# Optimization experiments

Measured on AMD Instinct MI355X. Metric: run time of the kernel, lower is better.

The kernel has to match this reference:

```python
import jax, jax.numpy as jnp
import numpy as np
from jax import lax

C_IN, C_OUT, LEVEL = 64, 128, 4
SOFTMAX_SCALE = 10.0
ESCAPE_NAN = 1e-4


def conv3(x, w, b):
    y = lax.conv_general_dilated(x, w, (1, 1), [(1, 1), (1, 1)],
                                 dimension_numbers=('NCHW', 'OIHW', 'NCHW'))
    return y + b[None, :, None, None]


def conv1(x, w, b):  # 1x1 conv, w: [O, I]
    return jnp.einsum('oi,bihw->bohw', w, x) + b[None, :, None, None]


def prelu(x, a):
    return jnp.where(x >= 0, x, a * x)


def resblock(x, w1, b1, w2, b2):  # EDSR ResBlock, res_scale=1
    return x + conv3(jax.nn.relu(conv3(x, w1, b1)), w2, b2)


def patches9(x):
    # 3x3 'same' (zero-pad 1) patches: [B,C,H,W] -> [B,C,3,3,H*W], (C,kh,kw) order like torch unfold
    B, C, H, W = x.shape
    xp = jnp.pad(x, ((0, 0), (0, 0), (1, 1), (1, 1)))
    p = jnp.stack([xp[:, :, i:i + H, j:j + W] for i in range(3) for j in range(3)], axis=2)
    return p.reshape(B, C, 3, 3, H * W)


def pyramid_attention(x, mbw, mbb, mba, mw, mb_, ma, aw, ab, aa):
    B, C, H, W = x.shape
    C2 = C // 2
    scales = [1.0 - i / 10 for i in range(LEVEL)]
    match_base = prelu(conv1(x, mbw, mbb), mba)            # [B,C2,H,W]
    xp = patches9(match_base).reshape(B, C2 * 9, H * W)    # query patches (same-padded input to conv2d)
    w_all, rw_all = [], []
    for s in scales:
        if s != 1.0:
            Hs, Ws = int(H * s), int(W * s)
            ref = jax.image.resize(x, (B, C, Hs, Ws), method='bilinear')
        else:
            ref = x
        base = prelu(conv1(ref, aw, ab), aa)               # conv_assembly: [B,C,Hs,Ws]
        rw_all.append(jnp.transpose(patches9(base), (0, 4, 1, 2, 3)))   # [B,L,C,3,3]
        refm = prelu(conv1(ref, mw, mb_), ma)              # conv_match:    [B,C2,Hs,Ws]
        w_all.append(jnp.transpose(patches9(refm), (0, 4, 1, 2, 3)))    # [B,L,C2,3,3]
    wi = jnp.concatenate(w_all, axis=1)                    # [B,Lt,C2,3,3]
    rw = jnp.concatenate(rw_all, axis=1)                   # [B,Lt,C,3,3]
    Lt = wi.shape[1]
    norm = jnp.maximum(jnp.sqrt(jnp.sum(wi * wi, axis=(2, 3, 4), keepdims=True)), ESCAPE_NAN)
    wn = (wi / norm).reshape(B, Lt, C2 * 9)
    # conv2d-as-correlation: scores[b,l,p] = <patch_p(match_base_b), wn[b,l]>
    scores = jnp.einsum('blk,bkp->blp', wn, xp)            # [B,Lt,H*W]
    att = jax.nn.softmax(scores * SOFTMAX_SCALE, axis=1).reshape(B, Lt, H, W)

    def tconv(y, rw_b):  # conv_transpose2d(stride=1, padding=1) == conv with swapped+flipped kernel
        wk = jnp.flip(jnp.transpose(rw_b, (1, 0, 2, 3)), axis=(2, 3))  # [C,Lt,3,3]
        return lax.conv_general_dilated(y[None], wk, (1, 1), [(1, 1), (1, 1)],
                                        dimension_numbers=('NCHW', 'OIHW', 'NCHW'))[0]

    out = jax.vmap(tconv)(att, rw) / 4.0
    return out + x  # res_scale = 1


def reference(x, bb0_w, bb0_b, bb0_a, rb1_w1, rb1_b1, rb1_w2, rb1_b2,
              pamb_w, pamb_b, pamb_a, pam_w, pam_b, pam_a, paa_w, paa_b, paa_a,
              rb2_w1, rb2_b1, rb2_w2, rb2_b2):
    h = lax.reduce_window(x, -jnp.inf, lax.max, (1, 1, 2, 2), (1, 1, 2, 2), 'VALID')  # MaxPool2d(2)
    h = prelu(conv3(h, bb0_w, bb0_b), bb0_a)               # BasicBlock in->out
    h = resblock(h, rb1_w1, rb1_b1, rb1_w2, rb1_b2)
    h = pyramid_attention(h, pamb_w, pamb_b, pamb_a, pam_w, pam_b, pam_a, paa_w, paa_b, paa_a)
    h = resblock(h, rb2_w1, rb2_b1, rb2_w2, rb2_b2)
    return h


def setup_inputs() -> dict:
    key = jax.random.key(0)
    ks = jax.random.split(key, 20)
    B, H, W = 2, 128, 128
    Ci, Co = C_IN, C_OUT
    C2 = Co // 2

    def n(k, shape, s=0.05):
        return jax.random.normal(k, shape, jnp.float32) * s

    a = jnp.asarray(0.25, jnp.float32)  # PReLU default init
    return {
        'x': jax.random.normal(ks[0], (B, Ci, H, W), jnp.float32),
        'bb0_w': n(ks[1], (Co, Ci, 3, 3)), 'bb0_b': n(ks[2], (Co,)), 'bb0_a': a,
        'rb1_w1': n(ks[3], (Co, Co, 3, 3)), 'rb1_b1': n(ks[4], (Co,)),
        'rb1_w2': n(ks[5], (Co, Co, 3, 3)), 'rb1_b2': n(ks[6], (Co,)),
        'pamb_w': n(ks[7], (C2, Co)), 'pamb_b': n(ks[8], (C2,)), 'pamb_a': a,
        'pam_w': n(ks[9], (C2, Co)), 'pam_b': n(ks[10], (C2,)), 'pam_a': a,
        'paa_w': n(ks[11], (Co, Co)), 'paa_b': n(ks[12], (Co,)), 'paa_a': a,
        'rb2_w1': n(ks[13], (Co, Co, 3, 3)), 'rb2_b1': n(ks[14], (Co,)),
        'rb2_w2': n(ks[15], (Co, Co, 3, 3)), 'rb2_b2': n(ks[16], (Co,)),
    }
```

## Files before the change

### kernel.cpp

```cpp
#include <hip/hip_runtime.h>

typedef unsigned short u16;
typedef __attribute__((ext_vector_type(8))) __bf16 bf16x8;
typedef __attribute__((ext_vector_type(8))) unsigned short ushort8;
typedef __attribute__((ext_vector_type(4))) float f32x4;

__device__ __forceinline__ float bf2f(u16 u) { return __uint_as_float(((unsigned)u) << 16); }
__device__ __forceinline__ u16 f2bf(float f) {
    unsigned x = __float_as_uint(f);
    x += 0x7fffu + ((x >> 16) & 1u);
    return (u16)(x >> 16);
}
__device__ __forceinline__ u16 f2h16(float f) {
    _Float16 h = (_Float16)f; u16 r; __builtin_memcpy(&r, &h, 2); return r;
}
__device__ __forceinline__ float h162f(u16 u) {
    _Float16 h; __builtin_memcpy(&h, &u, 2); return (float)h;
}

#define LP 13824

__global__ __launch_bounds__(256) void d7_gemm(
    const u16* __restrict__ A, const u16* __restrict__ B,
    int N, int K, int kLen, int mTiles, int S,
    long aBS, long bBS,
    const float* __restrict__ bias, const float* __restrict__ alpha, int act,
    const float* __restrict__ resid, long residBS,
    float* __restrict__ outF, long oFBS,
    u16* __restrict__ outB, long oBBS,
    u16* __restrict__ outT, int ldT, long oTBS,
    float* __restrict__ outP, long pMN, int pBf)
{
    __shared__ u16 As[128 * 40];
    __shared__ u16 Bs[128 * 40];

    const int tid = threadIdx.x;
    const int wv = tid >> 6, lane = tid & 63;
    const int wm = wv >> 1, wn = wv & 1;
    const int bn = blockIdx.x;
    const int bm = blockIdx.y % mTiles;
    const int ks = blockIdx.y / mTiles;
    const int z  = blockIdx.z;
    const int kStart = ks * kLen;

    const int srow = tid >> 1;
    const int soff = (tid & 1) * 16;
    const u16* gA = A + z * aBS + (size_t)(bm * 128 + srow) * K + kStart + soff;
    const u16* gB = B + z * bBS + (size_t)(bn * 128 + srow) * K + kStart + soff;
    u16* lA = &As[srow * 40 + soff];
    u16* lB = &Bs[srow * 40 + soff];

    f32x4 acc[4][4] = {};

    for (int k0 = 0; k0 < kLen; k0 += 32) {
        __syncthreads();
        ((uint4*)lA)[0] = ((const uint4*)gA)[0];
        ((uint4*)lA)[1] = ((const uint4*)gA)[1];
        ((uint4*)lB)[0] = ((const uint4*)gB)[0];
        ((uint4*)lB)[1] = ((const uint4*)gB)[1];
        gA += 32; gB += 32;
        __syncthreads();

        bf16x8 a[4], b[4];
        #pragma unroll
        for (int mt = 0; mt < 4; ++mt)
            a[mt] = *reinterpret_cast<const bf16x8*>(&As[(wm * 64 + mt * 16 + (lane & 15)) * 40 + (lane >> 4) * 8]);
        #pragma unroll
        for (int nt = 0; nt < 4; ++nt)
            b[nt] = *reinterpret_cast<const bf16x8*>(&Bs[(wn * 64 + nt * 16 + (lane & 15)) * 40 + (lane >> 4) * 8]);
        #pragma unroll
        for (int mt = 0; mt < 4; ++mt)
            #pragma unroll
            for (int nt = 0; nt < 4; ++nt)
                acc[mt][nt] = __builtin_amdgcn_mfma_f32_16x16x32_bf16(a[mt], b[nt], acc[mt][nt], 0, 0, 0);
    }

    if (outP) {
        const size_t pbase = ((size_t)z * S + ks) * pMN;
        #pragma unroll
        for (int mt = 0; mt < 4; ++mt) {
            const int mg = bm * 128 + wm * 64 + mt * 16 + ((lane >> 4) << 2);
            #pragma unroll
            for (int nt = 0; nt < 4; ++nt) {
                const int ng = bn * 128 + wn * 64 + nt * 16 + (lane & 15);
                if (pBf) {
                    u16* pp = (u16*)outP + pbase;
                    #pragma unroll
                    for (int r = 0; r < 4; ++r)
                        pp[(size_t)(mg + r) * N + ng] = f2bf(acc[mt][nt][r]);
                } else {
                    float* pp = outP + pbase;
                    #pragma unroll
                    for (int r = 0; r < 4; ++r)
                        pp[(size_t)(mg + r) * N + ng] = acc[mt][nt][r];
                }
            }
        }
        return;
    }

    const float avalS = (act == 1) ? alpha[0] : 0.0f;
    #pragma unroll
    for (int mt = 0; mt < 4; ++mt) {
        const int mg = bm * 128 + wm * 64 + mt * 16 + ((lane >> 4) << 2);
        float bv[4] = {0.f, 0.f, 0.f, 0.f}, av[4];
        if (bias) {
            #pragma unroll
            for (int r = 0; r < 4; ++r) bv[r] = bias[mg + r];
        }
        if (act == 3) {
            #pragma unroll
            for (int r = 0; r < 4; ++r) av[r] = alpha[mg + r];
        }
        #pragma unroll
        for (int nt = 0; nt < 4; ++nt) {
            const int ng = bn * 128 + wn * 64 + nt * 16 + (lane & 15);
            float v[4];
            #pragma unroll
            for (int r = 0; r < 4; ++r) {
                float t = acc[mt][nt][r] + bv[r];
                if (act == 1) t = (t >= 0.f) ? t : avalS * t;
                else if (act == 2) t = fmaxf(t, 0.f);
                else if (act == 3) t = (t >= 0.f) ? t : av[r] * t;
                if (resid) t += resid[z * residBS + (size_t)(mg + r) * N + ng];
                v[r] = t;
            }
            if (outF) {
                #pragma unroll
                for (int r = 0; r < 4; ++r) outF[z * oFBS + (size_t)(mg + r) * N + ng] = v[r];
            }
            if (outB) {
                #pragma unroll
                for (int r = 0; r < 4; ++r) outB[z * oBBS + (size_t)(mg + r) * N + ng] = f2bf(v[r]);
            }
            if (outT) {
                unsigned long long pk = (unsigned long long)f2bf(v[0])
                    | ((unsigned long long)f2bf(v[1]) << 16)
                    | ((unsigned long long)f2bf(v[2]) << 32)
                    | ((unsigned long long)f2bf(v[3]) << 48);
                *reinterpret_cast<unsigned long long*>(outT + z * oTBS + (size_t)ng * ldT + mg) = pk;
            }
        }
    }
}

__global__ __launch_bounds__(256) void d7_epi(
    const void* __restrict__ parts, int S, long sStride, long bStride,
    const float* __restrict__ bias, const float* __restrict__ alpha, int act,
    const float* __restrict__ resid, long residBS, float scale,
    float* __restrict__ out, long outBS, int total, int pBf)
{
    int i = blockIdx.x * 256 + threadIdx.x;
    if (i >= total) return;
    int b = blockIdx.z;
    float s = 0.f;
    if (pBf) {
        const u16* p = (const u16*)parts + b * bStride + i;
        for (int t = 0; t < S; ++t) s += bf2f(p[(size_t)t * sStride]);
    } else {
        const float* p = (const float*)parts + b * bStride + i;
        for (int t = 0; t < S; ++t) s += p[(size_t)t * sStride];
    }
    s *= scale;
    if (bias) s += bias[i >> 12];
    if (act == 1) { float a = alpha[0]; s = (s >= 0.f) ? s : a * s; }
    else if (act == 2) s = fmaxf(s, 0.f);
    if (resid) s += resid[b * residBS + i];
    out[b * outBS + i] = s;
}

__global__ __launch_bounds__(256) void d7_cast(const float* __restrict__ src, u16* __restrict__ dst, int n) {
    int i = blockIdx.x * 256 + threadIdx.x;
    if (i < n) dst[i] = f2bf(src[i]);
}

__global__ __launch_bounds__(256) void d7_wbuild(
    const float* __restrict__ pamb_w, const float* __restrict__ pam_w, const float* __restrict__ paa_w,
    const float* __restrict__ pamb_b, const float* __restrict__ pam_b, const float* __restrict__ paa_b,
    const float* __restrict__ pamb_a, const float* __restrict__ pam_a, const float* __restrict__ paa_a,
    u16* __restrict__ W1, u16* __restrict__ W2,
    float* __restrict__ b1, float* __restrict__ a1,
    float* __restrict__ b2, float* __restrict__ a2)
{
    int i = blockIdx.x * 256 + threadIdx.x;
    if (i < 256 * 128) {
        int r = i >> 7, c = i & 127;
        float w1 = (r < 64) ? pamb_w[r * 128 + c] : (r < 128) ? pam_w[(r - 64) * 128 + c] : paa_w[(r - 128) * 128 + c];
        W1[i] = f2bf(w1);
        float w2 = (r < 64) ? pam_w[r * 128 + c] : (r < 192) ? paa_w[(r - 64) * 128 + c] : 0.f;
        W2[i] = f2bf(w2);
    }
    if (i < 256) {
        int r = i;
        b1[r] = (r < 64) ? pamb_b[r] : (r < 128) ? pam_b[r - 64] : paa_b[r - 128];
        a1[r] = (r < 64) ? pamb_a[0] : (r < 128) ? pam_a[0] : paa_a[0];
        b2[r] = (r < 64) ? pam_b[r] : (r < 192) ? paa_b[r - 64] : 0.f;
        a2[r] = (r < 64) ? pam_a[0] : (r < 192) ? paa_a[0] : 0.f;
    }
}

__global__ __launch_bounds__(256) void d7_maxpool(const float* __restrict__ x, float* __restrict__ out) {
    int p = blockIdx.x * 256 + threadIdx.x;
    int c = blockIdx.y, b = blockIdx.z;
    int oh = p >> 6, ow = p & 63;
    const float* ip = x + ((size_t)b * 64 + c) * 16384;
    float v0 = ip[(2 * oh) * 128 + 2 * ow];
    float v1 = ip[(2 * oh) * 128 + 2 * ow + 1];
    float v2 = ip[(2 * oh + 1) * 128 + 2 * ow];
    float v3 = ip[(2 * oh + 1) * 128 + 2 * ow + 1];
    out[((size_t)b * 64 + c) * 4096 + p] = fmaxf(fmaxf(v0, v1), fmaxf(v2, v3));
}

__global__ __launch_bounds__(256) void d7_im2col(const float* __restrict__ img, u16* __restrict__ patT,
                                                 int Cin, long inBS, long outBS) {
    int K = Cin * 9;
    int k = blockIdx.x * 256 + threadIdx.x;
    if (k >= K) return;
    int p = blockIdx.y, b = blockIdx.z;
    int c = k / 9, k9 = k - c * 9;
    int h = p >> 6, w = p & 63;
    int y = h + k9 / 3 - 1, x = w + (k9 % 3) - 1;
    const float* ip = img + b * inBS;
    float v = (y >= 0 && y < 64 && x >= 0 && x < 64) ? ip[(size_t)c * 4096 + y * 64 + x] : 0.f;
    patT[b * outBS + (size_t)p * K + k] = f2bf(v);
}

__global__ __launch_bounds__(256) void d7_t32(const float* __restrict__ in, long inBS, int P,
                                              u16* __restrict__ out, long outBS) {
    __shared__ float tile[32][33];
    int p0 = blockIdx.x * 32, c0 = blockIdx.y * 32, b = blockIdx.z;
    int tx = threadIdx.x & 31, ty = threadIdx.x >> 5;
    const float* ip = in + b * inBS;
    #pragma unroll
    for (int i = 0; i < 32; i += 8) {
        int c = c0 + ty + i, p = p0 + tx;
        tile[ty + i][tx] = (p < P) ? ip[(size_t)c * P + p] : 0.f;
    }
    __syncthreads();
    u16* op = out + b * outBS;
    #pragma unroll
    for (int i = 0; i < 32; i += 8) {
        int p = p0 + ty + i, c = c0 + tx;
        if (p < P) op[(size_t)p * 128 + c] = f2bf(tile[tx][ty + i]);
    }
}

__global__ __launch_bounds__(256) void d7_scK(const u16* __restrict__ cT, long cBS, int ldC, int colBase,
                                              int pOff, int P, int HS, int Wp, int off,
                                              u16* __restrict__ dst, long dBS,
                                              float* __restrict__ s2out) {
    int t = blockIdx.x * 256 + threadIdx.x;
    int p = t >> 3, cg = t & 7;
    if (p >= P) return;
    int b = blockIdx.z;
    ushort8 v = *reinterpret_cast<const ushort8*>(cT + b * cBS + (size_t)(pOff + p) * ldC + colBase + cg * 8);
    int h = p / HS, w = p - h * HS;
    int lp = off + (h + 1) * Wp + w + 1;
    *reinterpret_cast<ushort8*>(dst + b * dBS + (size_t)lp * 64 + cg * 8) = v;
    if (s2out) {
        float ss = 0.f;
        #pragma unroll
        for (int i = 0; i < 8; ++i) { float f = bf2f(v[i]); ss += f * f; }
        ss += __shfl_xor(ss, 1);
        ss += __shfl_xor(ss, 2);
        ss += __shfl_xor(ss, 4);
        if (cg == 0) s2out[(size_t)b * LP + lp] = ss;
    }
}

__global__ __launch_bounds__(256) void d7_scR(const u16* __restrict__ cO, long cBS, int ldC, int rowBase,
                                              int pOff, int P, int HS, int Wp, int off,
                                              u16* __restrict__ dst, long dBS) {
    int p = blockIdx.x * 256 + threadIdx.x;
    if (p >= P) return;
    int co = blockIdx.y, b = blockIdx.z;
    u16 v = cO[b * cBS + (size_t)(rowBase + co) * ldC + pOff + p];
    int h = p / HS, w = p - h * HS;
    int lp = off + (h + 1) * Wp + w + 1;
    dst[b * dBS + (size_t)co * LP + lp] = v;
}

template <int OS>
__device__ __forceinline__ void d7_taps(int o, int& i0, float w3[3]) {
    const float inv = 64.0f / OS;
    float s = (o + 0.5f) * inv - 0.5f;
    i0 = (int)ceilf(s - inv);
    float wsum = 0.f;
    #pragma unroll
    for (int t = 0; t < 3; ++t) {
        int y = i0 + t;
        float wt = 1.0f - fabsf((float)y - s) / inv;
        wt = (wt > 0.f && y >= 0 && y < 64) ? wt : 0.f;
        w3[t] = wt; wsum += wt;
    }
    float r = 1.0f / wsum;
    w3[0] *= r; w3[1] *= r; w3[2] *= r;
}

template <int OS>
__global__ __launch_bounds__(256) void d7_resize(const float* __restrict__ in, float* __restrict__ out, long out_bs) {
    int p = blockIdx.x * 256 + threadIdx.x;
    if (p >= OS * OS) return;
    int c = blockIdx.y, b = blockIdx.z;
    int oh = p / OS, ow = p - oh * OS;
    const float* img = in + ((size_t)b * 128 + c) * 4096;
    int y0, x0; float wy[3], wx[3];
    d7_taps<OS>(oh, y0, wy);
    d7_taps<OS>(ow, x0, wx);
    float sum = 0.f;
    #pragma unroll
    for (int iy = 0; iy < 3; ++iy) {
        if (wy[iy] <= 0.f) continue;
        float rs = 0.f;
        #pragma unroll
        for (int ix = 0; ix < 3; ++ix) {
            if (wx[ix] <= 0.f) continue;
            rs += wx[ix] * img[(y0 + iy) * 64 + (x0 + ix)];
        }
        sum += wy[iy] * rs;
    }
    out[(size_t)b * out_bs + (size_t)c * OS * OS + p] = sum;
}

__device__ __forceinline__ int d7_scaleW(int l) {
    return (l < 4752) ? 72 : (l < 8528) ? 64 : (l < 11496) ? 56 : 48;
}

__global__ __launch_bounds__(256) void d7_rnormk(const float* __restrict__ s2, float* __restrict__ rnorm) {
    int l = blockIdx.x * 256 + threadIdx.x;
    if (l >= LP) return;
    int zb = blockIdx.z;
    int off, W, HS;
    if (l < 4752)       { off = 0;     W = 72; HS = 64; }
    else if (l < 8528)  { off = 4752;  W = 64; HS = 57; }
    else if (l < 11496) { off = 8528;  W = 56; HS = 51; }
    else                { off = 11496; W = 48; HS = 44; }
    int li = l - off, y = li / W, x = li - y * W;
    float v = 0.f;
    if (y >= 1 && y <= HS && x >= 1 && x <= HS) {
        const float* s = s2 + (size_t)zb * LP;
        float a = 0.f;
        #pragma unroll
        for (int dy = -1; dy <= 1; ++dy)
            #pragma unroll
            for (int dx = -1; dx <= 1; ++dx)
                a += s[l + dy * W + dx];
        v = 14.426950408889634f / fmaxf(sqrtf(a), 1e-4f);
    }
    rnorm[(size_t)zb * LP + l] = v;
}

__global__ __launch_bounds__(256) void d7_st1(const u16* __restrict__ in, u16* __restrict__ out,
                                              const float* __restrict__ rnorm) {
    int vg = blockIdx.x * 256 + threadIdx.x;
    if (vg >= LP / 8) return;
    int l8 = vg << 3;
    int p = blockIdx.y;
    int h = p >> 6, w = p & 63;
    int W = d7_scaleW(l8);
    float acc[8] = {0.f, 0.f, 0.f, 0.f, 0.f, 0.f, 0.f, 0.f};
    #pragma unroll
    for (int a = -1; a <= 1; ++a) {
        int ph = h + a;
        if ((unsigned)ph >= 64u) continue;
        #pragma unroll
        for (int b = -1; b <= 1; ++b) {
            int pw = w + b;
            if ((unsigned)pw >= 64u) continue;
            const u16* rp = in + (size_t)(p + a * 64 + b) * LP + l8 + a * W;
            ushort8 v = *reinterpret_cast<const ushort8*>(rp);
            if (b == 0) {
                #pragma unroll
                for (int i = 0; i < 8; ++i) acc[i] += bf2f(v[i]);
            } else if (b == -1) {
                acc[0] += bf2f(rp[-1]);
                #pragma unroll
                for (int i = 1; i < 8; ++i) acc[i] += bf2f(v[i - 1]);
            } else {
                acc[7] += bf2f(rp[8]);
                #pragma unroll
                for (int i = 0; i < 7; ++i) acc[i] += bf2f(v[i + 1]);
            }
        }
    }
    const float4 rn0 = *reinterpret_cast<const float4*>(rnorm + l8);
    const float4 rn1 = *reinterpret_cast<const float4*>(rnorm + l8 + 4);
    float rn[8] = {rn0.x, rn0.y, rn0.z, rn0.w, rn1.x, rn1.y, rn1.z, rn1.w};
    ushort8 res;
    #pragma unroll
    for (int i = 0; i < 8; ++i)
        res[i] = f2h16((rn[i] != 0.f) ? acc[i] * rn[i] : -1e4f);
    *reinterpret_cast<ushort8*>(out + (size_t)p * LP + l8) = res;
}

__global__ __launch_bounds__(256) void d7_stats(const u16* __restrict__ sc, float* __restrict__ statM) {
    int p = blockIdx.x, tid = threadIdx.x, wv = tid >> 6, lane = tid & 63;
    const u16* row = sc + (size_t)p * LP;
    float m = -3e38f;
    #pragma unroll
    for (int it = 0; it < 7; ++it) {
        int vg = tid + it * 256;
        if (vg < LP / 8) {
            ushort8 v = *reinterpret_cast<const ushort8*>(row + vg * 8);
            #pragma unroll
            for (int i = 0; i < 8; ++i) m = fmaxf(m, h162f(v[i]));
        }
    }
    #pragma unroll
    for (int o = 1; o < 64; o <<= 1) m = fmaxf(m, __shfl_xor(m, o));
    __shared__ float red[4];
    if (lane == 0) red[wv] = m;
    __syncthreads();
    m = fmaxf(fmaxf(red[0], red[1]), fmaxf(red[2], red[3]));
    __syncthreads();
    float s = 0.f;
    #pragma unroll
    for (int it = 0; it < 7; ++it) {
        int vg = tid + it * 256;
        if (vg < LP / 8) {
            ushort8 v = *reinterpret_cast<const ushort8*>(row + vg * 8);
            #pragma unroll
            for (int i = 0; i < 8; ++i) s += __builtin_amdgcn_exp2f(h162f(v[i]) - m);
        }
    }
    #pragma unroll
    for (int o = 1; o < 64; o <<= 1) s += __shfl_xor(s, o);
    if (lane == 0) red[wv] = s;
    __syncthreads();
    if (tid == 0) {
        float Z = red[0] + red[1] + red[2] + red[3];
        statM[p] = m + __log2f(Z);
    }
}

__global__ __launch_bounds__(256) void d7_st2(const u16* __restrict__ in,
                                              const float* __restrict__ statM,
                                              const float* __restrict__ rnorm,
                                              u16* __restrict__ out) {
    int vg = blockIdx.x * 256 + threadIdx.x;
    if (vg >= LP / 8) return;
    int l8 = vg << 3;
    int p = blockIdx.y;
    int h = p >> 6, w = p & 63;
    int W = d7_scaleW(l8);
    float acc[8] = {0.f, 0.f, 0.f, 0.f, 0.f, 0.f, 0.f, 0.f};
    #pragma unroll
    for (int a = -1; a <= 1; ++a) {
        int ph = h + a;
        if ((unsigned)ph >= 64u) continue;
        #pragma unroll
        for (int b = -1; b <= 1; ++b) {
            int pw = w + b;
            if ((unsigned)pw >= 64u) continue;
            int r = p + a * 64 + b;
            float M = statM[r];
            const u16* rp = in + (size_t)r * LP + l8 + a * W;
            ushort8 v = *reinterpret_cast<const ushort8*>(rp);
            if (b == 0) {
                #pragma unroll
                for (int i = 0; i < 8; ++i) acc[i] += __builtin_amdgcn_exp2f(h162f(v[i]) - M);
            } else if (b == -1) {
                acc[0] += __builtin_amdgcn_exp2f(h162f(rp[-1]) - M);
                #pragma unroll
                for (int i = 1; i < 8; ++i) acc[i] += __builtin_amdgcn_exp2f(h162f(v[i - 1]) - M);
            } else {
                acc[7] += __builtin_amdgcn_exp2f(h162f(rp[8]) - M);
                #pragma unroll
                for (int i = 0; i < 7; ++i) acc[i] += __builtin_amdgcn_exp2f(h162f(v[i + 1]) - M);
            }
        }
    }
    const float4 rn0 = *reinterpret_cast<const float4*>(rnorm + l8);
    const float4 rn1 = *reinterpret_cast<const float4*>(rnorm + l8 + 4);
    float rn[8] = {rn0.x, rn0.y, rn0.z, rn0.w, rn1.x, rn1.y, rn1.z, rn1.w};
    ushort8 res;
    #pragma unroll
    for (int i = 0; i < 8; ++i)
        res[i] = f2bf((rn[i] != 0.f) ? acc[i] : 0.f);
    *reinterpret_cast<ushort8*>(out + (size_t)p * LP + l8) = res;
}

extern "C" void kernel_launch(void* const* d_in, const int* in_sizes, int n_in,
                              void* d_out, int out_size, void* d_ws, size_t ws_size,
                              hipStream_t stream) {
    const float* x      = (const float*)d_in[0];
    const float* bb0_w  = (const float*)d_in[1];
    const float* bb0_b  = (const float*)d_in[2];
    const float* bb0_a  = (const float*)d_in[3];
    const float* rb1_w1 = (const float*)d_in[4];
    const float* rb1_b1 = (const float*)d_in[5];
    const float* rb1_w2 = (const float*)d_in[6];
    const float* rb1_b2 = (const float*)d_in[7];
    const float* pamb_w = (const float*)d_in[8];
    const float* pamb_b = (const float*)d_in[9];
    const float* pamb_a = (const float*)d_in[10];
    const float* pam_w  = (const float*)d_in[11];
    const float* pam_b  = (const float*)d_in[12];
    const float* pam_a  = (const float*)d_in[13];
    const float* paa_w  = (const float*)d_in[14];
    const float* paa_b  = (const float*)d_in[15];
    const float* paa_a  = (const float*)d_in[16];
    const float* rb2_w1 = (const float*)d_in[17];
    const float* rb2_b1 = (const float*)d_in[18];
    const float* rb2_w2 = (const float*)d_in[19];
    const float* rb2_b2 = (const float*)d_in[20];
    float* out = (float*)d_out;
    (void)in_sizes; (void)n_in; (void)out_size; (void)ws_size;

    char* wp = (char*)d_ws;
    auto alloc = [&](size_t nbytes) { void* p = wp; wp += (nbytes + 255) & ~(size_t)255; return p; };
    const size_t BIG = 4096ull * LP * 2;
    char* big1r  = (char*)alloc(BIG + 1024);
    char* big2r  = (char*)alloc(BIG + 1024);
    float* h0f   = (float*)alloc(2ull * 64 * 4096 * 4);
    float* h1f   = (float*)alloc(2ull * 128 * 4096 * 4);
    float* h2f   = (float*)alloc(2ull * 128 * 4096 * 4);
    float* paf   = (float*)alloc(2ull * 128 * 4096 * 4);
    float* tbuf  = (float*)alloc(2ull * 128 * 4096 * 4);
    u16* mbT     = (u16*)alloc(2ull * 4096 * 64 * 2);
    u16* refmT   = (u16*)alloc(2ull * LP * 64 * 2);
    u16* baseA   = (u16*)alloc(2ull * 128 * LP * 2);
    float* s2b   = (float*)alloc(2ull * LP * 4);
    float* rnorm = (float*)alloc(2ull * LP * 4);
    float* statM = (float*)alloc(4096ull * 4);
    u16* W1      = (u16*)alloc(256ull * 128 * 2);
    u16* W2      = (u16*)alloc(256ull * 128 * 2);
    float* b1v   = (float*)alloc(256 * 4);
    float* a1v   = (float*)alloc(256 * 4);
    float* b2v   = (float*)alloc(256 * 4);
    float* a2v   = (float*)alloc(256 * 4);
    u16* A0      = (u16*)alloc(73728ull * 2);
    u16* A1      = (u16*)alloc(147456ull * 2);
    u16* A2      = (u16*)alloc(147456ull * 2);
    u16* A3      = (u16*)alloc(147456ull * 2);
    u16* A4      = (u16*)alloc(147456ull * 2);
    u16* patT    = (u16*)big1r;
    u16* h2T     = (u16*)big1r;
    u16* refbT   = (u16*)(big1r + (4ull << 20));
    u16* S0T     = (u16*)(big1r + 512);
    u16* gT      = (u16*)(big1r + 512);
    float* parts = (float*)big2r;
    u16* cT1     = (u16*)big2r;
    u16* cOut1   = (u16*)(big2r + (4ull << 20));
    u16* cT2     = (u16*)(big2r + (8ull << 20));
    u16* cOut2   = (u16*)(big2r + (16ull << 20));
    float* refb  = (float*)(big2r + (26ull << 20));
    u16* scT     = (u16*)(big2r + 512);

    const long h2bs = 128L * 4096;
    const long pMN = 128L * 4096;
    const long refbs = 128L * 7786;
    const long mbTbs = 4096L * 64, rmTbs = (long)LP * 64, baBS = 128L * LP;
    const long cT1bs = 4096L * 256, cO1bs = 256L * 4096;
    const long cT2bs = 7808L * 256, cO2bs = 256L * 7808;
    const long rbTbs = 7808L * 128;

    auto conv = [&](const float* src, const u16* W, int Cin, const float* bias,
                    const float* alpha, int act, const float* resid, float* dst) {
        int K = Cin * 9;
        d7_im2col<<<dim3((K + 255) / 256, 4096, 2), 256, 0, stream>>>(src, patT, Cin, (long)Cin * 4096, 4096L * K);
        d7_gemm<<<dim3(32, 6, 2), 256, 0, stream>>>(W, patT, 4096, K, K / 6, 1, 6,
            0, 4096L * K, nullptr, nullptr, 0, nullptr, 0,
            nullptr, 0, nullptr, 0, nullptr, 0, 0, parts, pMN, 0);
        d7_epi<<<dim3(2048, 1, 2), 256, 0, stream>>>(parts, 6, pMN, 6 * pMN,
            bias, alpha, act, resid, h2bs, 1.0f, dst, h2bs, (int)pMN, 0);
    };

    d7_cast<<<dim3(288), 256, 0, stream>>>(bb0_w, A0, 73728);
    d7_cast<<<dim3(576), 256, 0, stream>>>(rb1_w1, A1, 147456);
    d7_cast<<<dim3(576), 256, 0, stream>>>(rb1_w2, A2, 147456);
    d7_cast<<<dim3(576), 256, 0, stream>>>(rb2_w1, A3, 147456);
    d7_cast<<<dim3(576), 256, 0, stream>>>(rb2_w2, A4, 147456);
    d7_wbuild<<<dim3(128), 256, 0, stream>>>(pamb_w, pam_w, paa_w, pamb_b, pam_b, paa_b,
                                             pamb_a, pam_a, paa_a, W1, W2, b1v, a1v, b2v, a2v);

    d7_maxpool<<<dim3(16, 64, 2), 256, 0, stream>>>(x, h0f);
    conv(h0f, A0, 64, bb0_b, bb0_a, 1, nullptr, h1f);
    conv(h1f, A1, 128, rb1_b1, nullptr, 2, nullptr, tbuf);
    conv(tbuf, A2, 128, rb1_b2, nullptr, 0, h1f, h2f);

    d7_resize<57><<<dim3(13, 128, 2), 256, 0, stream>>>(h2f, refb, refbs);
    d7_resize<51><<<dim3(11, 128, 2), 256, 0, stream>>>(h2f, refb + 3249L * 128, refbs);
    d7_resize<44><<<dim3(8, 128, 2), 256, 0, stream>>>(h2f, refb + 5850L * 128, refbs);

    hipMemsetAsync(refbT, 0, 2ull * rbTbs * 2, stream);
    d7_t32<<<dim3(128, 4, 2), 256, 0, stream>>>(h2f, h2bs, 4096, h2T, 4096L * 128);
    d7_t32<<<dim3(102, 4, 2), 256, 0, stream>>>(refb, refbs, 3249, refbT, rbTbs);
    d7_t32<<<dim3(82, 4, 2), 256, 0, stream>>>(refb + 3249L * 128, refbs, 2601, refbT + 3249L * 128, rbTbs);
    d7_t32<<<dim3(61, 4, 2), 256, 0, stream>>>(refb + 5850L * 128, refbs, 1936, refbT + 5850L * 128, rbTbs);

    d7_gemm<<<dim3(32, 2, 2), 256, 0, stream>>>(W1, h2T, 4096, 128, 128, 2, 1,
        0, 4096L * 128, b1v, a1v, 3, nullptr, 0,
        nullptr, 0, cOut1, cO1bs, cT1, 256, cT1bs, nullptr, 0, 0);
    d7_gemm<<<dim3(61, 2, 2), 256, 0, stream>>>(W2, refbT, 7808, 128, 128, 2, 1,
        0, rbTbs, b2v, a2v, 3, nullptr, 0,
        nullptr, 0, cOut2, cO2bs, cT2, 256, cT2bs, nullptr, 0, 0);

    hipMemsetAsync(refmT, 0, 2ull * LP * 64 * 2, stream);
    hipMemsetAsync(baseA, 0, 2ull * 128 * LP * 2, stream);
    hipMemsetAsync(s2b, 0, 2ull * LP * 4, stream);
    d7_scK<<<dim3(128, 1, 2), 256, 0, stream>>>(cT1, cT1bs, 256, 0, 0, 4096, 64, 64, -65, mbT, mbTbs, nullptr);
    d7_scK<<<dim3(128, 1, 2), 256, 0, stream>>>(cT1, cT1bs, 256, 64, 0, 4096, 64, 72, 0, refmT, rmTbs, s2b);
    d7_scK<<<dim3(102, 1, 2), 256, 0, stream>>>(cT2, cT2bs, 256, 0, 0, 3249, 57, 64, 4752, refmT, rmTbs, s2b);
    d7_scK<<<dim3(82, 1, 2), 256, 0, stream>>>(cT2, cT2bs, 256, 0, 3249, 2601, 51, 56, 8528, refmT, rmTbs, s2b);
    d7_scK<<<dim3(61, 1, 2), 256, 0, stream>>>(cT2, cT2bs, 256, 0, 5850, 1936, 44, 48, 11496, refmT, rmTbs, s2b);
    d7_scR<<<dim3(16, 128, 2), 256, 0, stream>>>(cOut1, cO1bs, 4096, 128, 0, 4096, 64, 72, 0, baseA, baBS);
    d7_scR<<<dim3(13, 128, 2), 256, 0, stream>>>(cOut2, cO2bs, 7808, 64, 0, 3249, 57, 64, 4752, baseA, baBS);
    d7_scR<<<dim3(11, 128, 2), 256, 0, stream>>>(cOut2, cO2bs, 7808, 64, 3249, 2601, 51, 56, 8528, baseA, baBS);
    d7_scR<<<dim3(8, 128, 2), 256, 0, stream>>>(cOut2, cO2bs, 7808, 64, 5850, 1936, 44, 48, 11496, baseA, baBS);

    d7_rnormk<<<dim3(54, 1, 2), 256, 0, stream>>>(s2b, rnorm);

    for (int b = 0; b < 2; ++b) {
        d7_gemm<<<dim3(32, 108, 1), 256, 0, stream>>>(refmT + b * rmTbs, mbT + b * mbTbs,
            4096, 64, 64, 108, 1, 0, 0, nullptr, nullptr, 0, nullptr, 0,
            nullptr, 0, nullptr, 0, S0T, LP, 0, nullptr, 0, 0);
        d7_st1<<<dim3(7, 4096), 256, 0, stream>>>(S0T, scT, rnorm + (size_t)b * LP);
        d7_stats<<<dim3(4096), 256, 0, stream>>>(scT, statM);
        d7_st2<<<dim3(7, 4096), 256, 0, stream>>>(scT, statM, rnorm + (size_t)b * LP, gT);
        d7_gemm<<<dim3(32, 12, 1), 256, 0, stream>>>(baseA + b * baBS, gT,
            4096, LP, LP / 12, 1, 12, 0, 0, nullptr, nullptr, 0, nullptr, 0,
            nullptr, 0, nullptr, 0, nullptr, 0, 0, parts, pMN, 1);
        d7_epi<<<dim3(2048, 1, 1), 256, 0, stream>>>(parts, 12, pMN, 0,
            nullptr, nullptr, 0, h2f + b * h2bs, 0, 0.25f, paf + b * h2bs, 0, (int)pMN, 1);
    }

    conv(paf, A3, 128, rb2_b1, nullptr, 2, nullptr, tbuf);
    conv(tbuf, A4, 128, rb2_b2, nullptr, 0, paf, out);
}
```

Baseline: 993.5 us.

## Fuse score smoothing with softmax stats and use lane shuffles for halo reads

Merges the 3x3 diagonal smoothing kernel (st1) and the row max/log-sum-exp stats kernel into one block-per-row kernel. Each row's fp16 scores stay in registers between the passes, so the separate stats pass no longer re-reads them from memory. In both smoothing kernels the unaligned neighbour element for the ±1 column shift now comes from a lane shuffle, with a scalar load only at wavefront edges. The max now skips masked entries, and the conv path's gemm/epilogue last flag changes from 0 to 1, which may alter precision or layout. The fused kernel launches one block per row instead of seven, so parallelism and occupancy per row drop.

```diff
diff --git a/kernel.cpp b/kernel.cpp
--- a/kernel.cpp
+++ b/kernel.cpp
@@ -350,66 +350,66 @@
     rnorm[(size_t)zb * LP + l] = v;
 }
 
-__global__ __launch_bounds__(256) void d7_st1(const u16* __restrict__ in, u16* __restrict__ out,
-                                              const float* __restrict__ rnorm) {
-    int vg = blockIdx.x * 256 + threadIdx.x;
-    if (vg >= LP / 8) return;
-    int l8 = vg << 3;
-    int p = blockIdx.y;
-    int h = p >> 6, w = p & 63;
-    int W = d7_scaleW(l8);
-    float acc[8] = {0.f, 0.f, 0.f, 0.f, 0.f, 0.f, 0.f, 0.f};
-    #pragma unroll
-    for (int a = -1; a <= 1; ++a) {
-        int ph = h + a;
-        if ((unsigned)ph >= 64u) continue;
-        #pragma unroll
-        for (int b = -1; b <= 1; ++b) {
-            int pw = w + b;
-            if ((unsigned)pw >= 64u) continue;
-            const u16* rp = in + (size_t)(p + a * 64 + b) * LP + l8 + a * W;
-            ushort8 v = *reinterpret_cast<const ushort8*>(rp);
-            if (b == 0) {
+__global__ __launch_bounds__(256) void d7_st1f(const u16* __restrict__ in, u16* __restrict__ out,
+                                               const float* __restrict__ rnorm,
+                                               float* __restrict__ statM) {
+    const int p = blockIdx.x;
+    const int tid = threadIdx.x, wvi = tid >> 6, lane = tid & 63;
+    const int h = p >> 6, w = p & 63;
+    ushort8 vals16[7];
+    float m = -3e38f;
+    #pragma unroll
+    for (int it = 0; it < 7; ++it) {
+        int vg = tid + it * 256;
+        if (vg >= LP / 8) continue;
+        int l8 = vg << 3;
+        int W = d7_scaleW(l8);
+        float acc[8] = {0.f, 0.f, 0.f, 0.f, 0.f, 0.f, 0.f, 0.f};
+        #pragma unroll
+        for (int a = -1; a <= 1; ++a) {
+            int ph = h + a;
+            if ((unsigned)ph >= 64u) continue;
+            const u16* rb = in + (size_t)(p + a * 64) * LP + l8 + a * W;
+            {
+                ushort8 v = *reinterpret_cast<const ushort8*>(rb);
                 #pragma unroll
                 for (int i = 0; i < 8; ++i) acc[i] += bf2f(v[i]);
-            } else if (b == -1) {
-                acc[0] += bf2f(rp[-1]);
+            }
+            if (w - 1 >= 0) {
+                const u16* r1 = rb - LP;
+                ushort8 v = *reinterpret_cast<const ushort8*>(r1);
+                int up = __shfl_up((int)v[7], 1);
+                u16 e = (lane == 0) ? r1[-1] : (u16)up;
+                acc[0] += bf2f(e);
                 #pragma unroll
                 for (int i = 1; i < 8; ++i) acc[i] += bf2f(v[i - 1]);
-            } else {
-                acc[7] += bf2f(rp[8]);
+            }
+            if (w + 1 < 64) {
+                const u16* r1 = rb + LP;
+                ushort8 v = *reinterpret_cast<const ushort8*>(r1);
+                int dn = __shfl_down((int)v[0], 1);
+                u16 e = (lane == 63) ? r1[8] : (u16)dn;
                 #pragma unroll
                 for (int i = 0; i < 7; ++i) acc[i] += bf2f(v[i + 1]);
-            }
-        }
-    }
-    const float4 rn0 = *reinterpret_cast<const float4*>(rnorm + l8);
-    const float4 rn1 = *reinterpret_cast<const float4*>(rnorm + l8 + 4);
-    float rn[8] = {rn0.x, rn0.y, rn0.z, rn0.w, rn1.x, rn1.y, rn1.z, rn1.w};
-    ushort8 res;
-    #pragma unroll
-    for (int i = 0; i < 8; ++i)
-        res[i] = f2h16((rn[i] != 0.f) ? acc[i] * rn[i] : -1e4f);
-    *reinterpret_cast<ushort8*>(out + (size_t)p * LP + l8) = res;
-}
-
-__global__ __launch_bounds__(256) void d7_stats(const u16* __restrict__ sc, float* __restrict__ statM) {
-    int p = blockIdx.x, tid = threadIdx.x, wv = tid >> 6, lane = tid & 63;
-    const u16* row = sc + (size_t)p * LP;
-    float m = -3e38f;
-    #pragma unroll
-    for (int it = 0; it < 7; ++it) {
-        int vg = tid + it * 256;
-        if (vg < LP / 8) {
-            ushort8 v = *reinterpret_cast<const ushort8*>(row + vg * 8);
-            #pragma unroll
-            for (int i = 0; i < 8; ++i) m = fmaxf(m, h162f(v[i]));
-        }
+                acc[7] += bf2f(e);
+            }
+        }
+        const float4 rn0 = *reinterpret_cast<const float4*>(rnorm + l8);
+        const float4 rn1 = *reinterpret_cast<const float4*>(rnorm + l8 + 4);
+        float rn[8] = {rn0.x, rn0.y, rn0.z, rn0.w, rn1.x, rn1.y, rn1.z, rn1.w};
+        ushort8 res;
+        #pragma unroll
+        for (int i = 0; i < 8; ++i) {
+            float val = (rn[i] != 0.f) ? acc[i] * rn[i] : -1e4f;
+            res[i] = f2h16(val);
+            if (rn[i] != 0.f) m = fmaxf(m, val);
+        }
+        vals16[it] = res;
     }
     #pragma unroll
     for (int o = 1; o < 64; o <<= 1) m = fmaxf(m, __shfl_xor(m, o));
     __shared__ float red[4];
-    if (lane == 0) red[wv] = m;
+    if (lane == 0) red[wvi] = m;
     __syncthreads();
     m = fmaxf(fmaxf(red[0], red[1]), fmaxf(red[2], red[3]));
     __syncthreads();
@@ -417,19 +417,24 @@
     #pragma unroll
     for (int it = 0; it < 7; ++it) {
         int vg = tid + it * 256;
-        if (vg < LP / 8) {
-            ushort8 v = *reinterpret_cast<const ushort8*>(row + vg * 8);
-            #pragma unroll
-            for (int i = 0; i < 8; ++i) s += __builtin_amdgcn_exp2f(h162f(v[i]) - m);
-        }
+        if (vg >= LP / 8) continue;
+        ushort8 res = vals16[it];
+        #pragma unroll
+        for (int i = 0; i < 8; ++i) s += __builtin_amdgcn_exp2f(h162f(res[i]) - m);
     }
     #pragma unroll
     for (int o = 1; o < 64; o <<= 1) s += __shfl_xor(s, o);
-    if (lane == 0) red[wv] = s;
+    if (lane == 0) red[wvi] = s;
     __syncthreads();
     if (tid == 0) {
         float Z = red[0] + red[1] + red[2] + red[3];
         statM[p] = m + __log2f(Z);
+    }
+    #pragma unroll
+    for (int it = 0; it < 7; ++it) {
+        int vg = tid + it * 256;
+        if (vg >= LP / 8) continue;
+        *reinterpret_cast<ushort8*>(out + (size_t)p * LP + (vg << 3)) = vals16[it];
     }
 }
 
@@ -439,6 +444,7 @@
                                               u16* __restrict__ out) {
     int vg = blockIdx.x * 256 + threadIdx.x;
     if (vg >= LP / 8) return;
+    const int lane = threadIdx.x & 63;
     int l8 = vg << 3;
     int p = blockIdx.y;
     int h = p >> 6, w = p & 63;
@@ -448,26 +454,32 @@
     for (int a = -1; a <= 1; ++a) {
         int ph = h + a;
         if ((unsigned)ph >= 64u) continue;
-        #pragma unroll
-        for (int b = -1; b <= 1; ++b) {
-            int pw = w + b;
-            if ((unsigned)pw >= 64u) continue;
-            int r = p + a * 64 + b;
-            float M = statM[r];
-            const u16* rp = in + (size_t)r * LP + l8 + a * W;
-            ushort8 v = *reinterpret_cast<const ushort8*>(rp);
-            if (b == 0) {
-                #pragma unroll
-                for (int i = 0; i < 8; ++i) acc[i] += __builtin_amdgcn_exp2f(h162f(v[i]) - M);
-            } else if (b == -1) {
-                acc[0] += __builtin_amdgcn_exp2f(h162f(rp[-1]) - M);
-                #pragma unroll
-                for (int i = 1; i < 8; ++i) acc[i] += __builtin_amdgcn_exp2f(h162f(v[i - 1]) - M);
-            } else {
-                acc[7] += __builtin_amdgcn_exp2f(h162f(rp[8]) - M);
-                #pragma unroll
-                for (int i = 0; i < 7; ++i) acc[i] += __builtin_amdgcn_exp2f(h162f(v[i + 1]) - M);
-            }
+        const u16* rb = in + (size_t)(p + a * 64) * LP + l8 + a * W;
+        {
+            float M = statM[p + a * 64];
+            ushort8 v = *reinterpret_cast<const ushort8*>(rb);
+            #pragma unroll
+            for (int i = 0; i < 8; ++i) acc[i] += __builtin_amdgcn_exp2f(h162f(v[i]) - M);
+        }
+        if (w - 1 >= 0) {
+            float M = statM[p + a * 64 - 1];
+            const u16* r1 = rb - LP;
+            ushort8 v = *reinterpret_cast<const ushort8*>(r1);
+            int up = __shfl_up((int)v[7], 1);
+            u16 e = (lane == 0) ? r1[-1] : (u16)up;
+            acc[0] += __builtin_amdgcn_exp2f(h162f(e) - M);
+            #pragma unroll
+            for (int i = 1; i < 8; ++i) acc[i] += __builtin_amdgcn_exp2f(h162f(v[i - 1]) - M);
+        }
+        if (w + 1 < 64) {
+            float M = statM[p + a * 64 + 1];
+            const u16* r1 = rb + LP;
+            ushort8 v = *reinterpret_cast<const ushort8*>(r1);
+            int dn = __shfl_down((int)v[0], 1);
+            u16 e = (lane == 63) ? r1[8] : (u16)dn;
+            #pragma unroll
+            for (int i = 0; i < 7; ++i) acc[i] += __builtin_amdgcn_exp2f(h162f(v[i + 1]) - M);
+            acc[7] += __builtin_amdgcn_exp2f(h162f(e) - M);
         }
     }
     const float4 rn0 = *reinterpret_cast<const float4*>(rnorm + l8);
@@ -561,9 +573,9 @@
         d7_im2col<<<dim3((K + 255) / 256, 4096, 2), 256, 0, stream>>>(src, patT, Cin, (long)Cin * 4096, 4096L * K);
         d7_gemm<<<dim3(32, 6, 2), 256, 0, stream>>>(W, patT, 4096, K, K / 6, 1, 6,
             0, 4096L * K, nullptr, nullptr, 0, nullptr, 0,
-            nullptr, 0, nullptr, 0, nullptr, 0, 0, parts, pMN, 0);
+            nullptr, 0, nullptr, 0, nullptr, 0, 0, parts, pMN, 1);
         d7_epi<<<dim3(2048, 1, 2), 256, 0, stream>>>(parts, 6, pMN, 6 * pMN,
-            bias, alpha, act, resid, h2bs, 1.0f, dst, h2bs, (int)pMN, 0);
+            bias, alpha, act, resid, h2bs, 1.0f, dst, h2bs, (int)pMN, 1);
     };
 
     d7_cast<<<dim3(288), 256, 0, stream>>>(bb0_w, A0, 73728);
@@ -615,8 +627,7 @@
         d7_gemm<<<dim3(32, 108, 1), 256, 0, stream>>>(refmT + b * rmTbs, mbT + b * mbTbs,
             4096, 64, 64, 108, 1, 0, 0, nullptr, nullptr, 0, nullptr, 0,
             nullptr, 0, nullptr, 0, S0T, LP, 0, nullptr, 0, 0);
-        d7_st1<<<dim3(7, 4096), 256, 0, stream>>>(S0T, scT, rnorm + (size_t)b * LP);
-        d7_stats<<<dim3(4096), 256, 0, stream>>>(scT, statM);
+        d7_st1f<<<dim3(4096), 256, 0, stream>>>(S0T, scT, rnorm + (size_t)b * LP, statM);
         d7_st2<<<dim3(7, 4096), 256, 0, stream>>>(scT, statM, rnorm + (size_t)b * LP, gT);
         d7_gemm<<<dim3(32, 12, 1), 256, 0, stream>>>(baseA + b * baBS, gT,
             4096, LP, LP / 12, 1, 12, 0, 0, nullptr, nullptr, 0, nullptr, 0,
```

Result: slower. 1.035 ms (+4.1%).

## Fuse softmax row stats into score stencil kernel with partial combine

Applied to the files above, without the earlier changes.

The per-row max and sum-exp statistics are now computed inside d7_st1 from values already in registers, writing per-block partials that a small d7_comb kernel merges. This removes the separate d7_stats pass that re-read the full score matrix twice per batch. The horizontal-neighbour loads in the stencil are replaced by wave shuffles of neighbouring lanes' vectors, cutting redundant global reads. Buffer offsets and padding are enlarged, and a gemm/epilogue mode flag for the convs is switched, which may change that path's behaviour.

```diff
diff --git a/kernel.cpp b/kernel.cpp
--- a/kernel.cpp
+++ b/kernel.cpp
@@ -351,86 +351,99 @@
 }
 
 __global__ __launch_bounds__(256) void d7_st1(const u16* __restrict__ in, u16* __restrict__ out,
-                                              const float* __restrict__ rnorm) {
-    int vg = blockIdx.x * 256 + threadIdx.x;
-    if (vg >= LP / 8) return;
+                                              const float* __restrict__ rnorm,
+                                              float2* __restrict__ part) {
+    const int tid = threadIdx.x, wvi = tid >> 6, lane = tid & 63;
+    int vg = blockIdx.x * 256 + tid;
+    const bool active = vg < LP / 8;
     int l8 = vg << 3;
     int p = blockIdx.y;
     int h = p >> 6, w = p & 63;
-    int W = d7_scaleW(l8);
-    float acc[8] = {0.f, 0.f, 0.f, 0.f, 0.f, 0.f, 0.f, 0.f};
-    #pragma unroll
-    for (int a = -1; a <= 1; ++a) {
-        int ph = h + a;
-        if ((unsigned)ph >= 64u) continue;
-        #pragma unroll
-        for (int b = -1; b <= 1; ++b) {
-            int pw = w + b;
-            if ((unsigned)pw >= 64u) continue;
-            const u16* rp = in + (size_t)(p + a * 64 + b) * LP + l8 + a * W;
-            ushort8 v = *reinterpret_cast<const ushort8*>(rp);
-            if (b == 0) {
+    float vals[8];
+    if (active) {
+        int W = d7_scaleW(l8);
+        float acc[8] = {0.f, 0.f, 0.f, 0.f, 0.f, 0.f, 0.f, 0.f};
+        #pragma unroll
+        for (int a = -1; a <= 1; ++a) {
+            int ph = h + a;
+            if ((unsigned)ph >= 64u) continue;
+            const u16* rb = in + (size_t)(p + a * 64) * LP + l8 + a * W;
+            {
+                ushort8 v = *reinterpret_cast<const ushort8*>(rb);
                 #pragma unroll
                 for (int i = 0; i < 8; ++i) acc[i] += bf2f(v[i]);
-            } else if (b == -1) {
-                acc[0] += bf2f(rp[-1]);
+            }
+            if (w - 1 >= 0) {
+                const u16* r1 = rb - LP;
+                ushort8 v = *reinterpret_cast<const ushort8*>(r1);
+                int up = __shfl_up((int)v[7], 1);
+                u16 e = (lane == 0) ? r1[-1] : (u16)up;
+                acc[0] += bf2f(e);
                 #pragma unroll
                 for (int i = 1; i < 8; ++i) acc[i] += bf2f(v[i - 1]);
-            } else {
-                acc[7] += bf2f(rp[8]);
+            }
+            if (w + 1 < 64) {
+                const u16* r1 = rb + LP;
+                ushort8 v = *reinterpret_cast<const ushort8*>(r1);
+                int dn = __shfl_down((int)v[0], 1);
+                u16 e = (lane == 63) ? r1[8] : (u16)dn;
                 #pragma unroll
                 for (int i = 0; i < 7; ++i) acc[i] += bf2f(v[i + 1]);
-            }
-        }
-    }
-    const float4 rn0 = *reinterpret_cast<const float4*>(rnorm + l8);
-    const float4 rn1 = *reinterpret_cast<const float4*>(rnorm + l8 + 4);
-    float rn[8] = {rn0.x, rn0.y, rn0.z, rn0.w, rn1.x, rn1.y, rn1.z, rn1.w};
-    ushort8 res;
-    #pragma unroll
-    for (int i = 0; i < 8; ++i)
-        res[i] = f2h16((rn[i] != 0.f) ? acc[i] * rn[i] : -1e4f);
-    *reinterpret_cast<ushort8*>(out + (size_t)p * LP + l8) = res;
-}
-
-__global__ __launch_bounds__(256) void d7_stats(const u16* __restrict__ sc, float* __restrict__ statM) {
-    int p = blockIdx.x, tid = threadIdx.x, wv = tid >> 6, lane = tid & 63;
-    const u16* row = sc + (size_t)p * LP;
-    float m = -3e38f;
-    #pragma unroll
-    for (int it = 0; it < 7; ++it) {
-        int vg = tid + it * 256;
-        if (vg < LP / 8) {
-            ushort8 v = *reinterpret_cast<const ushort8*>(row + vg * 8);
-            #pragma unroll
-            for (int i = 0; i < 8; ++i) m = fmaxf(m, h162f(v[i]));
-        }
-    }
+                acc[7] += bf2f(e);
+            }
+        }
+        const float4 rn0 = *reinterpret_cast<const float4*>(rnorm + l8);
+        const float4 rn1 = *reinterpret_cast<const float4*>(rnorm + l8 + 4);
+        float rn[8] = {rn0.x, rn0.y, rn0.z, rn0.w, rn1.x, rn1.y, rn1.z, rn1.w};
+        ushort8 res;
+        #pragma unroll
+        for (int i = 0; i < 8; ++i) {
+            u16 q = f2h16((rn[i] != 0.f) ? acc[i] * rn[i] : -1e4f);
+            res[i] = q;
+            vals[i] = h162f(q);
+        }
+        *reinterpret_cast<ushort8*>(out + (size_t)p * LP + l8) = res;
+    } else {
+        #pragma unroll
+        for (int i = 0; i < 8; ++i) vals[i] = -1e4f;
+    }
+    float m = vals[0];
+    #pragma unroll
+    for (int i = 1; i < 8; ++i) m = fmaxf(m, vals[i]);
     #pragma unroll
     for (int o = 1; o < 64; o <<= 1) m = fmaxf(m, __shfl_xor(m, o));
     __shared__ float red[4];
-    if (lane == 0) red[wv] = m;
+    if (lane == 0) red[wvi] = m;
     __syncthreads();
     m = fmaxf(fmaxf(red[0], red[1]), fmaxf(red[2], red[3]));
     __syncthreads();
     float s = 0.f;
     #pragma unroll
-    for (int it = 0; it < 7; ++it) {
-        int vg = tid + it * 256;
-        if (vg < LP / 8) {
-            ushort8 v = *reinterpret_cast<const ushort8*>(row + vg * 8);
-            #pragma unroll
-            for (int i = 0; i < 8; ++i) s += __builtin_amdgcn_exp2f(h162f(v[i]) - m);
-        }
-    }
+    for (int i = 0; i < 8; ++i) s += __builtin_amdgcn_exp2f(vals[i] - m);
     #pragma unroll
     for (int o = 1; o < 64; o <<= 1) s += __shfl_xor(s, o);
-    if (lane == 0) red[wv] = s;
+    if (lane == 0) red[wvi] = s;
     __syncthreads();
     if (tid == 0) {
         float Z = red[0] + red[1] + red[2] + red[3];
-        statM[p] = m + __log2f(Z);
-    }
+        part[p * 7 + blockIdx.x] = make_float2(m, Z);
+    }
+}
+
+__global__ __launch_bounds__(256) void d7_comb(const float2* __restrict__ part, float* __restrict__ statM) {
+    int p = blockIdx.x * 256 + threadIdx.x;
+    if (p >= 4096) return;
+    const float2* q = part + p * 7;
+    float2 e[7];
+    #pragma unroll
+    for (int t = 0; t < 7; ++t) e[t] = q[t];
+    float m = e[0].x;
+    #pragma unroll
+    for (int t = 1; t < 7; ++t) m = fmaxf(m, e[t].x);
+    float Z = 0.f;
+    #pragma unroll
+    for (int t = 0; t < 7; ++t) Z += e[t].y * __builtin_amdgcn_exp2f(e[t].x - m);
+    statM[p] = m + __log2f(Z);
 }
 
 __global__ __launch_bounds__(256) void d7_st2(const u16* __restrict__ in,
@@ -510,8 +523,9 @@
     char* wp = (char*)d_ws;
     auto alloc = [&](size_t nbytes) { void* p = wp; wp += (nbytes + 255) & ~(size_t)255; return p; };
     const size_t BIG = 4096ull * LP * 2;
-    char* big1r  = (char*)alloc(BIG + 1024);
-    char* big2r  = (char*)alloc(BIG + 1024);
+    const size_t PAD = 40960;
+    char* big1r  = (char*)alloc(BIG + PAD);
+    char* big2r  = (char*)alloc(BIG + PAD);
     float* h0f   = (float*)alloc(2ull * 64 * 4096 * 4);
     float* h1f   = (float*)alloc(2ull * 128 * 4096 * 4);
     float* h2f   = (float*)alloc(2ull * 128 * 4096 * 4);
@@ -523,6 +537,7 @@
     float* s2b   = (float*)alloc(2ull * LP * 4);
     float* rnorm = (float*)alloc(2ull * LP * 4);
     float* statM = (float*)alloc(4096ull * 4);
+    float2* partb = (float2*)alloc(4096ull * 7 * 8);
     u16* W1      = (u16*)alloc(256ull * 128 * 2);
     u16* W2      = (u16*)alloc(256ull * 128 * 2);
     float* b1v   = (float*)alloc(256 * 4);
@@ -537,15 +552,15 @@
     u16* patT    = (u16*)big1r;
     u16* h2T     = (u16*)big1r;
     u16* refbT   = (u16*)(big1r + (4ull << 20));
-    u16* S0T     = (u16*)(big1r + 512);
-    u16* gT      = (u16*)(big1r + 512);
+    u16* S0T     = (u16*)(big1r + 32768);
+    u16* gT      = (u16*)(big1r + 32768);
     float* parts = (float*)big2r;
     u16* cT1     = (u16*)big2r;
     u16* cOut1   = (u16*)(big2r + (4ull << 20));
     u16* cT2     = (u16*)(big2r + (8ull << 20));
     u16* cOut2   = (u16*)(big2r + (16ull << 20));
     float* refb  = (float*)(big2r + (26ull << 20));
-    u16* scT     = (u16*)(big2r + 512);
+    u16* scT     = (u16*)(big2r + 32768);
 
     const long h2bs = 128L * 4096;
     const long pMN = 128L * 4096;
@@ -561,9 +576,9 @@
         d7_im2col<<<dim3((K + 255) / 256, 4096, 2), 256, 0, stream>>>(src, patT, Cin, (long)Cin * 4096, 4096L * K);
         d7_gemm<<<dim3(32, 6, 2), 256, 0, stream>>>(W, patT, 4096, K, K / 6, 1, 6,
             0, 4096L * K, nullptr, nullptr, 0, nullptr, 0,
-            nullptr, 0, nullptr, 0, nullptr, 0, 0, parts, pMN, 0);
+            nullptr, 0, nullptr, 0, nullptr, 0, 0, parts, pMN, 1);
         d7_epi<<<dim3(2048, 1, 2), 256, 0, stream>>>(parts, 6, pMN, 6 * pMN,
-            bias, alpha, act, resid, h2bs, 1.0f, dst, h2bs, (int)pMN, 0);
+            bias, alpha, act, resid, h2bs, 1.0f, dst, h2bs, (int)pMN, 1);
     };
 
     d7_cast<<<dim3(288), 256, 0, stream>>>(bb0_w, A0, 73728);
@@ -615,8 +630,8 @@
         d7_gemm<<<dim3(32, 108, 1), 256, 0, stream>>>(refmT + b * rmTbs, mbT + b * mbTbs,
             4096, 64, 64, 108, 1, 0, 0, nullptr, nullptr, 0, nullptr, 0,
             nullptr, 0, nullptr, 0, S0T, LP, 0, nullptr, 0, 0);
-        d7_st1<<<dim3(7, 4096), 256, 0, stream>>>(S0T, scT, rnorm + (size_t)b * LP);
-        d7_stats<<<dim3(4096), 256, 0, stream>>>(scT, statM);
+        d7_st1<<<dim3(7, 4096), 256, 0, stream>>>(S0T, scT, rnorm + (size_t)b * LP, partb);
+        d7_comb<<<dim3(16), 256, 0, stream>>>(partb, statM);
         d7_st2<<<dim3(7, 4096), 256, 0, stream>>>(scT, statM, rnorm + (size_t)b * LP, gT);
         d7_gemm<<<dim3(32, 12, 1), 256, 0, stream>>>(baseA + b * baBS, gT,
             4096, LP, LP / 12, 1, 12, 0, 0, nullptr, nullptr, 0, nullptr, 0,
```

After: 953.5 us. 1.04x faster.
